# Kernel tuning notes

Measured on AMD Instinct MI355X. Metric: run time of the kernel, lower is better.

## Reference

```python
import jax, jax.numpy as jnp
import numpy as np

N = 16384
IN_DIM = 512
HID = 256
E = 262144


def setup_inputs() -> dict:
    key = jax.random.key(0)
    k1, k2, k3, k4, k5, k6 = jax.random.split(key, 6)
    # Xavier-uniform-like init scale for the weights
    lim1 = float(np.sqrt(6.0 / (IN_DIM + HID)))
    lim2 = float(np.sqrt(6.0 / (HID + 1)))
    return {
        "X": jax.random.normal(k1, (N, IN_DIM), dtype=jnp.float32),
        "adj": jax.random.uniform(k2, (N, N), dtype=jnp.float32),
        "weight": jax.random.uniform(k3, (IN_DIM, HID), dtype=jnp.float32, minval=-lim1, maxval=lim1),
        "weight_two": jax.random.uniform(k4, (HID, 1), dtype=jnp.float32, minval=-lim2, maxval=lim2),
        "train_edges": jax.random.randint(k5, (E, 2), 0, N, dtype=jnp.int64 if jax.config.read("jax_enable_x64") else jnp.int32),
        "train_false_edges": jax.random.randint(k6, (E, 2), 0, N, dtype=jnp.int64 if jax.config.read("jax_enable_x64") else jnp.int32),
    }


def reference(X, adj, weight, weight_two, train_edges, train_false_edges):
    # encode: Z = adj @ (X @ W)
    Z = adj @ (X @ weight)  # [N, HID]
    # decode: per-edge gather + elementwise multiply + small linear + sigmoid
    edges = jnp.concatenate([train_edges, train_false_edges], axis=0)  # [2E, 2]
    z_i = Z[edges[:, 0]]  # [2E, HID]
    z_j = Z[edges[:, 1]]  # [2E, HID]
    logits = (z_i * z_j) @ weight_two  # [2E, 1]
    return jax.nn.sigmoid(logits)
```

## Files before the change

kernel.cpp:

```cpp
#include <hip/hip_runtime.h>
#include <math.h>


typedef _Float16 half8v __attribute__((ext_vector_type(8)));
typedef __attribute__((ext_vector_type(4))) float floatx4;

#define NM_ (16384L * 256L)
#define KT 256

static __device__ __forceinline__ void split2_pair_f16(float x0, float x1,
                                                       unsigned& q1, unsigned& q2) {
  _Float16 h0 = (_Float16)x0, h1 = (_Float16)x1;
  float r0 = x0 - (float)h0, r1 = x1 - (float)h1;
  _Float16 g0 = (_Float16)r0, g1 = (_Float16)r1;
  q1 = ((unsigned)__builtin_bit_cast(unsigned short, h1) << 16) |
       __builtin_bit_cast(unsigned short, h0);
  q2 = ((unsigned)__builtin_bit_cast(unsigned short, g1) << 16) |
       __builtin_bit_cast(unsigned short, g0);
}

#define BM 128
#define BN 128
#define BK 16
#define LDAS (BM + 4)
#define LDBS (BN + 4)

__global__ __launch_bounds__(256, 1)
void gemm_f32_nn(const float* __restrict__ A, const float* __restrict__ B,
                 float* __restrict__ C, int M, int N, int K)
{
  __shared__ float As[2][BK][LDAS];
  __shared__ float Bs[2][BK][LDBS];

  const int tid = threadIdx.x;
  const int tx = tid & 15;
  const int ty = tid >> 4;
  const long m0 = (long)blockIdx.x * BM;
  const long n0 = (long)blockIdx.y * BN;

  const int a_row = tid >> 2;
  const int a_kc  = (tid & 3) << 2;
  const int b_row = tid >> 5;
  const int b_col = (tid & 31) << 2;

  const float* Ag0 = A + (m0 + a_row) * (long)K + a_kc;
  const float* Ag1 = A + (m0 + 64 + a_row) * (long)K + a_kc;
  const float* Bg0 = B + (long)b_row * N + n0 + b_col;
  const float* Bg1 = B + (long)(b_row + 8) * N + n0 + b_col;

  float4 av0 = *(const float4*)(Ag0);
  float4 av1 = *(const float4*)(Ag1);
  float4 bv0 = *(const float4*)(Bg0);
  float4 bv1 = *(const float4*)(Bg1);

  float acc[8][8];
#pragma unroll
  for (int i = 0; i < 8; ++i)
#pragma unroll
    for (int j = 0; j < 8; ++j) acc[i][j] = 0.f;

  const int nt = K / BK;
  int buf = 0;

#pragma unroll
  for (int i = 0; i < 4; ++i) {
    As[0][a_kc + i][a_row]      = (&av0.x)[i];
    As[0][a_kc + i][a_row + 64] = (&av1.x)[i];
  }
  *(float4*)&Bs[0][b_row][b_col]     = bv0;
  *(float4*)&Bs[0][b_row + 8][b_col] = bv1;
  __syncthreads();

  for (int t = 0; t < nt; ++t) {
    if (t + 1 < nt) {
      const long ko = (long)(t + 1) * BK;
      av0 = *(const float4*)(Ag0 + ko);
      av1 = *(const float4*)(Ag1 + ko);
      bv0 = *(const float4*)(Bg0 + ko * N);
      bv1 = *(const float4*)(Bg1 + ko * N);
    }
    float tacc[8][8];
#pragma unroll
    for (int i = 0; i < 8; ++i)
#pragma unroll
      for (int j = 0; j < 8; ++j) tacc[i][j] = 0.f;

#pragma unroll
    for (int kk = 0; kk < BK; ++kk) {
      float4 aA = *(const float4*)&As[buf][kk][ty * 4];
      float4 aB = *(const float4*)&As[buf][kk][ty * 4 + 64];
      float4 bA = *(const float4*)&Bs[buf][kk][tx * 4];
      float4 bB = *(const float4*)&Bs[buf][kk][tx * 4 + 64];
      const float ar[8] = {aA.x, aA.y, aA.z, aA.w, aB.x, aB.y, aB.z, aB.w};
      const float br[8] = {bA.x, bA.y, bA.z, bA.w, bB.x, bB.y, bB.z, bB.w};
#pragma unroll
      for (int i = 0; i < 8; ++i)
#pragma unroll
        for (int j = 0; j < 8; ++j)
          tacc[i][j] = fmaf(ar[i], br[j], tacc[i][j]);
    }
#pragma unroll
    for (int i = 0; i < 8; ++i)
#pragma unroll
      for (int j = 0; j < 8; ++j) acc[i][j] += tacc[i][j];

    if (t + 1 < nt) {
      const int nb = buf ^ 1;
#pragma unroll
      for (int i = 0; i < 4; ++i) {
        As[nb][a_kc + i][a_row]      = (&av0.x)[i];
        As[nb][a_kc + i][a_row + 64] = (&av1.x)[i];
      }
      *(float4*)&Bs[nb][b_row][b_col]     = bv0;
      *(float4*)&Bs[nb][b_row + 8][b_col] = bv1;
    }
    __syncthreads();
    buf ^= 1;
  }

#pragma unroll
  for (int i = 0; i < 8; ++i) {
    const long row = m0 + (i < 4 ? ty * 4 + i : 64 + ty * 4 + (i - 4));
#pragma unroll
    for (int c = 0; c < 2; ++c) {
      float4 v;
      v.x = acc[i][c * 4 + 0];
      v.y = acc[i][c * 4 + 1];
      v.z = acc[i][c * 4 + 2];
      v.w = acc[i][c * 4 + 3];
      *(float4*)&C[row * N + n0 + tx * 4 + c * 64] = v;
    }
  }
}

__global__ __launch_bounds__(256)
void transpose_split(const float* __restrict__ XW,
                     unsigned short* __restrict__ X1,
                     unsigned short* __restrict__ X2)
{
  __shared__ float T[64][65];
  const int tid = threadIdx.x;
  const long kb = (long)blockIdx.x * 64;
  const long nb = (long)blockIdx.y * 64;

#pragma unroll
  for (int i = 0; i < 4; ++i) {
    int idx = tid + 256 * i;
    int r = idx >> 4, c4 = (idx & 15) * 4;
    float4 v = *(const float4*)&XW[(kb + r) * 256 + nb + c4];
    T[r][c4 + 0] = v.x; T[r][c4 + 1] = v.y; T[r][c4 + 2] = v.z; T[r][c4 + 3] = v.w;
  }
  __syncthreads();

#pragma unroll
  for (int i = 0; i < 2; ++i) {
    int idx = tid + 256 * i;
    int n = idx >> 3, kq = (idx & 7) * 8;
    float x[8];
#pragma unroll
    for (int j = 0; j < 8; ++j) x[j] = T[kq + j][n];
    unsigned q1[4], q2[4];
#pragma unroll
    for (int p = 0; p < 4; ++p)
      split2_pair_f16(x[2 * p], x[2 * p + 1], q1[p], q2[p]);
    const long gk = kb + kq;
    const long gt = gk >> 5;
    const int  c  = (int)((gk >> 3) & 3);
    const long o  = ((gt * 4 + c) * 256 + (nb + n)) * 8;
    *(uint4*)&X1[o] = make_uint4(q1[0], q1[1], q1[2], q1[3]);
    *(uint4*)&X2[o] = make_uint4(q2[0], q2[1], q2[2], q2[3]);
  }
}


__global__ __launch_bounds__(256, 2)
void gemm_split2(const float* __restrict__ A,
                 const unsigned short* __restrict__ Bg,
                 float* __restrict__ P0, float* __restrict__ P1)
{
  __shared__ unsigned short As[2][8192];

  const int tid  = threadIdx.x;
  const int lane = tid & 63;
  const int w    = tid >> 6;
  const int wm   = w >> 1, wn = w & 1;

  const int bid = blockIdx.x;
  const int swz = (bid & 7) * 64 + (bid >> 3);
  const long m0 = (long)(swz >> 2) * 128;
  const long n0 = (long)((swz >> 1) & 1) * 128;
  const int  z  = swz & 1;
  float* __restrict__ Cp = z ? P1 : P0;

  const int arow = tid & 127;
  const int ah   = tid >> 7;
  const float* Ag = A + (m0 + arow) * 16384L + (long)z * 8192 + ah * 16;

  int awr[2][2];
#pragma unroll
  for (int s = 0; s < 2; ++s)
#pragma unroll
    for (int q = 0; q < 2; ++q)
      awr[s][q] = ((s * 4 + 2 * ah + q) * 128 + arow) * 8;

  const int fr = lane & 15;
  const int kc = lane >> 4;

  const unsigned short* Bq = Bg + (long)kc * 2048 + ((long)n0 + wn * 64 + fr) * 8;

  floatx4 acc[4][4], accS[4][4];
#pragma unroll
  for (int i = 0; i < 4; ++i)
#pragma unroll
    for (int j = 0; j < 4; ++j) { acc[i][j] = (floatx4)0.f; accS[i][j] = (floatx4)0.f; }

  float4  pa[4];
  half8v  bf[2][4];

#define SPLIT_WRITE(NB)                                                           \
  {                                                                               \
    unsigned q1[8], q2[8];                                                        \
    _Pragma("unroll")                                                             \
    for (int p = 0; p < 8; ++p) {                                                 \
      float x0 = (&pa[p >> 1].x)[(2 * p) & 3];                                    \
      float x1 = (&pa[p >> 1].x)[(2 * p + 1) & 3];                                \
      split2_pair_f16(x0, x1, q1[p], q2[p]);                                      \
    }                                                                             \
    *(uint4*)&As[NB][awr[0][0]] = make_uint4(q1[0], q1[1], q1[2], q1[3]);         \
    *(uint4*)&As[NB][awr[0][1]] = make_uint4(q1[4], q1[5], q1[6], q1[7]);         \
    *(uint4*)&As[NB][awr[1][0]] = make_uint4(q2[0], q2[1], q2[2], q2[3]);         \
    *(uint4*)&As[NB][awr[1][1]] = make_uint4(q2[4], q2[5], q2[6], q2[7]);         \
  }

#define LOAD_BF(TILE)                                                             \
  {                                                                               \
    const long bo_ = ((long)z * KT + (TILE)) * 8192;                              \
    _Pragma("unroll")                                                             \
    for (int s = 0; s < 2; ++s)                                                   \
      _Pragma("unroll")                                                           \
      for (int fn = 0; fn < 4; ++fn)                                              \
        bf[s][fn] = *(const half8v*)(Bq + s * NM_ + bo_ + fn * 128);              \
  }

#define BODY(TT, CUR)                                                             \
  {                                                                               \
    SPLIT_WRITE((CUR) ^ 1);                                                       \
    {                                                                             \
      const long ko_ = (long)(((TT) + 2) & (KT - 1)) * 32;                        \
      _Pragma("unroll")                                                           \
      for (int i = 0; i < 4; ++i) pa[i] = *(const float4*)(Ag + ko_ + i * 4);     \
    }                                                                             \
    _Pragma("unroll")                                                             \
    for (int fm = 0; fm < 4; ++fm) {                                              \
      const int ar_ = (wm * 64 + fm * 16 + fr) * 8;                               \
      half8v af0 = *(const half8v*)&As[CUR][kc * 1024 + ar_];                     \
      half8v af1 = *(const half8v*)&As[CUR][(4 + kc) * 1024 + ar_];               \
      _Pragma("unroll")                                                           \
      for (int fn = 0; fn < 4; ++fn) {                                            \
        floatx4 d = acc[fm][fn];                                                  \
        d = __builtin_amdgcn_mfma_f32_16x16x32_f16(af0, bf[0][fn], d, 0, 0, 0);   \
        d = __builtin_amdgcn_mfma_f32_16x16x32_f16(af0, bf[1][fn], d, 0, 0, 0);   \
        d = __builtin_amdgcn_mfma_f32_16x16x32_f16(af1, bf[0][fn], d, 0, 0, 0);   \
        acc[fm][fn] = d;                                                          \
      }                                                                           \
    }                                                                             \
    LOAD_BF(((TT) + 1) & (KT - 1));                                               \
    if (((TT) & 31) == 31) {                                                      \
      _Pragma("unroll")                                                           \
      for (int i = 0; i < 4; ++i)                                                 \
        _Pragma("unroll")                                                         \
        for (int j = 0; j < 4; ++j) { accS[i][j] += acc[i][j]; acc[i][j] = (floatx4)0.f; } \
    }                                                                             \
    asm volatile("s_waitcnt lgkmcnt(0)" ::: "memory");                            \
    __builtin_amdgcn_s_barrier();                                                 \
    __builtin_amdgcn_sched_barrier(0);                                            \
  }

#pragma unroll
  for (int i = 0; i < 4; ++i) pa[i] = *(const float4*)(Ag + i * 4);
  LOAD_BF(0);
  SPLIT_WRITE(0);
#pragma unroll
  for (int i = 0; i < 4; ++i) pa[i] = *(const float4*)(Ag + 32 + i * 4);
  asm volatile("s_waitcnt lgkmcnt(0)" ::: "memory");
  __builtin_amdgcn_s_barrier();
  __builtin_amdgcn_sched_barrier(0);

  for (int t = 0; t < KT; t += 2) {
    BODY(t,     0);
    BODY(t + 1, 1);
  }

#pragma unroll
  for (int fm = 0; fm < 4; ++fm) {
#pragma unroll
    for (int fn = 0; fn < 4; ++fn) {
      const long col  = n0 + wn * 64 + fn * 16 + fr;
      const long rowb = m0 + wm * 64 + fm * 16 + (lane >> 4) * 4;
#pragma unroll
      for (int j = 0; j < 4; ++j)
        Cp[(rowb + j) * 256 + col] = accS[fm][fn][j];
    }
  }
#undef BODY
#undef LOAD_BF
#undef SPLIT_WRITE
}

__global__ __launch_bounds__(256)
void reduce_add(const float* __restrict__ P0, float* __restrict__ P1, long n4)
{
  long i = (long)blockIdx.x * 256 + threadIdx.x;
  const long stride = (long)gridDim.x * 256;
  for (; i < n4; i += stride) {
    float4 a = ((const float4*)P0)[i];
    float4 b = ((const float4*)P1)[i];
    b.x += a.x; b.y += a.y; b.z += a.z; b.w += a.w;
    ((float4*)P1)[i] = b;
  }
}

__global__ __launch_bounds__(256)
void edge_score(const float* __restrict__ Z, const float* __restrict__ w2,
                const int* __restrict__ te, const int* __restrict__ fe,
                int E, float* __restrict__ out)
{
  const long gtid = (long)blockIdx.x * 256 + threadIdx.x;
  const long wid = gtid >> 6;
  const int lane = threadIdx.x & 63;
  if (wid >= 2L * E) return;
  const int* ep = (wid < E) ? (te + 2 * wid) : (fe + 2 * (wid - E));
  const int src = ep[0];
  const int dst = ep[1];
  const float4 a = ((const float4*)(Z + (long)src * 256))[lane];
  const float4 b = ((const float4*)(Z + (long)dst * 256))[lane];
  const float4 w = ((const float4*)w2)[lane];
  float s = a.x * b.x * w.x + a.y * b.y * w.y + a.z * b.z * w.z + a.w * b.w * w.w;
#pragma unroll
  for (int off = 32; off > 0; off >>= 1) s += __shfl_down(s, off);
  if (lane == 0) out[wid] = 1.0f / (1.0f + expf(-s));
}

extern "C" void kernel_launch(void* const* d_in, const int* in_sizes, int n_in,
                              void* d_out, int out_size, void* d_ws, size_t ws_size,
                              hipStream_t stream)
{
  const float* X   = (const float*)d_in[0];
  const float* adj = (const float*)d_in[1];
  const float* W   = (const float*)d_in[2];
  const float* W2  = (const float*)d_in[3];
  const int*   te  = (const int*)d_in[4];
  const int*   fe  = (const int*)d_in[5];

  const int E = in_sizes[4] / 2;

  float* ws = (float*)d_ws;
  float* XW = ws;
  float* P0 = ws;
  float* P1 = ws + NM_;
  unsigned short* X1 = (unsigned short*)(ws + 2 * NM_);
  unsigned short* X2 = X1 + NM_;

  dim3 blk(256);
  gemm_f32_nn<<<dim3(128, 2), blk, 0, stream>>>(X, W, XW, 16384, 256, 512);
  transpose_split<<<dim3(256, 4), blk, 0, stream>>>(XW, X1, X2);
  gemm_split2<<<dim3(512), blk, 0, stream>>>(adj, X1, P0, P1);
  reduce_add<<<dim3(2048), blk, 0, stream>>>(P0, P1, NM_ / 4);
  const long nwaves = 2L * E;
  const int nblocks = (int)((nwaves + 3) / 4);
  edge_score<<<dim3(nblocks), blk, 0, stream>>>(P1, W2, te, fe, E, (float*)d_out);
}
```

Measured before the change: 767.2 us.

## Use split-fp16 MFMA for X@W and restructure adj GEMM without LDS

Replaces the FP32 SIMT GEMM for X@W with a split-fp16 MFMA kernel, fed by a new kernel that pre-splits W into hi/lo fp16 halves. The adj GEMM is rebuilt so each 512-thread block covers all 256 output columns. Each wave loads and splits its own A fragments directly from global memory into registers, with no LDS staging or barriers. This removes shared-memory traffic and syncs and reads each adj row tile once per K-half. The trade-off is that lanes load A fragments with strided, less coalesced accesses, and register pressure rises.

```diff
diff --git a/kernel.cpp b/kernel.cpp
--- a/kernel.cpp
+++ b/kernel.cpp
@@ -3,10 +3,10 @@
 
 
 typedef _Float16 half8v __attribute__((ext_vector_type(8)));
+typedef __fp16   fp16x2 __attribute__((ext_vector_type(2)));
 typedef __attribute__((ext_vector_type(4))) float floatx4;
 
 #define NM_ (16384L * 256L)
-#define KT 256
 
 static __device__ __forceinline__ void split2_pair_f16(float x0, float x1,
                                                        unsigned& q1, unsigned& q2) {
@@ -19,118 +19,99 @@
        __builtin_bit_cast(unsigned short, g0);
 }
 
-#define BM 128
-#define BN 128
-#define BK 16
-#define LDAS (BM + 4)
-#define LDBS (BN + 4)
-
-__global__ __launch_bounds__(256, 1)
-void gemm_f32_nn(const float* __restrict__ A, const float* __restrict__ B,
-                 float* __restrict__ C, int M, int N, int K)
-{
-  __shared__ float As[2][BK][LDAS];
-  __shared__ float Bs[2][BK][LDBS];
-
-  const int tid = threadIdx.x;
-  const int tx = tid & 15;
-  const int ty = tid >> 4;
-  const long m0 = (long)blockIdx.x * BM;
-  const long n0 = (long)blockIdx.y * BN;
-
-  const int a_row = tid >> 2;
-  const int a_kc  = (tid & 3) << 2;
-  const int b_row = tid >> 5;
-  const int b_col = (tid & 31) << 2;
-
-  const float* Ag0 = A + (m0 + a_row) * (long)K + a_kc;
-  const float* Ag1 = A + (m0 + 64 + a_row) * (long)K + a_kc;
-  const float* Bg0 = B + (long)b_row * N + n0 + b_col;
-  const float* Bg1 = B + (long)(b_row + 8) * N + n0 + b_col;
-
-  float4 av0 = *(const float4*)(Ag0);
-  float4 av1 = *(const float4*)(Ag1);
-  float4 bv0 = *(const float4*)(Bg0);
-  float4 bv1 = *(const float4*)(Bg1);
-
-  float acc[8][8];
-#pragma unroll
-  for (int i = 0; i < 8; ++i)
-#pragma unroll
-    for (int j = 0; j < 8; ++j) acc[i][j] = 0.f;
-
-  const int nt = K / BK;
-  int buf = 0;
-
-#pragma unroll
-  for (int i = 0; i < 4; ++i) {
-    As[0][a_kc + i][a_row]      = (&av0.x)[i];
-    As[0][a_kc + i][a_row + 64] = (&av1.x)[i];
-  }
-  *(float4*)&Bs[0][b_row][b_col]     = bv0;
-  *(float4*)&Bs[0][b_row + 8][b_col] = bv1;
-  __syncthreads();
-
-  for (int t = 0; t < nt; ++t) {
-    if (t + 1 < nt) {
-      const long ko = (long)(t + 1) * BK;
-      av0 = *(const float4*)(Ag0 + ko);
-      av1 = *(const float4*)(Ag1 + ko);
-      bv0 = *(const float4*)(Bg0 + ko * N);
-      bv1 = *(const float4*)(Bg1 + ko * N);
-    }
-    float tacc[8][8];
-#pragma unroll
-    for (int i = 0; i < 8; ++i)
-#pragma unroll
-      for (int j = 0; j < 8; ++j) tacc[i][j] = 0.f;
-
-#pragma unroll
-    for (int kk = 0; kk < BK; ++kk) {
-      float4 aA = *(const float4*)&As[buf][kk][ty * 4];
-      float4 aB = *(const float4*)&As[buf][kk][ty * 4 + 64];
-      float4 bA = *(const float4*)&Bs[buf][kk][tx * 4];
-      float4 bB = *(const float4*)&Bs[buf][kk][tx * 4 + 64];
-      const float ar[8] = {aA.x, aA.y, aA.z, aA.w, aB.x, aB.y, aB.z, aB.w};
-      const float br[8] = {bA.x, bA.y, bA.z, bA.w, bB.x, bB.y, bB.z, bB.w};
-#pragma unroll
-      for (int i = 0; i < 8; ++i)
-#pragma unroll
-        for (int j = 0; j < 8; ++j)
-          tacc[i][j] = fmaf(ar[i], br[j], tacc[i][j]);
-    }
-#pragma unroll
-    for (int i = 0; i < 8; ++i)
-#pragma unroll
-      for (int j = 0; j < 8; ++j) acc[i][j] += tacc[i][j];
-
-    if (t + 1 < nt) {
-      const int nb = buf ^ 1;
-#pragma unroll
-      for (int i = 0; i < 4; ++i) {
-        As[nb][a_kc + i][a_row]      = (&av0.x)[i];
-        As[nb][a_kc + i][a_row + 64] = (&av1.x)[i];
+static __device__ __forceinline__ void split8(const float* __restrict__ x,
+                                              half8v& a0, half8v& a1) {
+  union U { unsigned u[4]; half8v h; } u0, u1;
+#pragma unroll
+  for (int p = 0; p < 4; ++p) {
+    fp16x2 h = __builtin_amdgcn_cvt_pkrtz(x[2 * p], x[2 * p + 1]);
+    float r0 = x[2 * p]     - (float)h[0];
+    float r1 = x[2 * p + 1] - (float)h[1];
+    fp16x2 g = __builtin_amdgcn_cvt_pkrtz(r0, r1);
+    u0.u[p] = __builtin_bit_cast(unsigned, h);
+    u1.u[p] = __builtin_bit_cast(unsigned, g);
+  }
+  a0 = u0.h; a1 = u1.h;
+}
+
+__global__ __launch_bounds__(256)
+void w_split(const float* __restrict__ W, unsigned short* __restrict__ WT)
+{
+  const int b  = blockIdx.x;
+  const int kt = b >> 2, c = b & 3;
+  const int n  = threadIdx.x;
+  const int k0 = kt * 32 + c * 8;
+  float x[8];
+#pragma unroll
+  for (int j = 0; j < 8; ++j) x[j] = W[(k0 + j) * 256 + n];
+  unsigned q1[4], q2[4];
+#pragma unroll
+  for (int p = 0; p < 4; ++p)
+    split2_pair_f16(x[2 * p], x[2 * p + 1], q1[p], q2[p]);
+  const long o = ((long)(kt * 4 + c) * 256 + n) * 8;
+  *(uint4*)&WT[o]          = make_uint4(q1[0], q1[1], q1[2], q1[3]);
+  *(uint4*)&WT[o + 131072] = make_uint4(q2[0], q2[1], q2[2], q2[3]);
+}
+
+__global__ __launch_bounds__(256, 2)
+void gemm_xw(const float* __restrict__ X, const unsigned short* __restrict__ WT,
+             float* __restrict__ XW)
+{
+  const int tid  = threadIdx.x;
+  const int lane = tid & 63;
+  const int w    = tid >> 6;
+  const int wm = w >> 1, wn = w & 1;
+  const long m0 = (long)(blockIdx.x >> 1) * 128;
+  const long n0 = (long)(blockIdx.x & 1) * 128;
+  const int fr = lane & 15, kc = lane >> 4;
+
+  const unsigned short* Bq = WT + (long)kc * 2048 + ((long)n0 + wn * 64 + fr) * 8;
+
+  const float* ap[4];
+#pragma unroll
+  for (int fm = 0; fm < 4; ++fm)
+    ap[fm] = X + (m0 + wm * 64 + fm * 16 + fr) * 512L + kc * 8;
+
+  floatx4 acc[4][4];
+#pragma unroll
+  for (int i = 0; i < 4; ++i)
+#pragma unroll
+    for (int j = 0; j < 4; ++j) acc[i][j] = (floatx4)0.f;
+
+  for (int t = 0; t < 16; ++t) {
+    half8v bf0[4], bf1[4];
+#pragma unroll
+    for (int fn = 0; fn < 4; ++fn) {
+      bf0[fn] = *(const half8v*)(Bq + (long)t * 8192 + fn * 128);
+      bf1[fn] = *(const half8v*)(Bq + (long)t * 8192 + fn * 128 + 131072);
+    }
+#pragma unroll
+    for (int fm = 0; fm < 4; ++fm) {
+      float x[8];
+      *(float4*)&x[0] = *(const float4*)(ap[fm] + t * 32);
+      *(float4*)&x[4] = *(const float4*)(ap[fm] + t * 32 + 4);
+      half8v a0, a1;
+      split8(x, a0, a1);
+#pragma unroll
+      for (int fn = 0; fn < 4; ++fn) {
+        floatx4 d = acc[fm][fn];
+        d = __builtin_amdgcn_mfma_f32_16x16x32_f16(a0, bf0[fn], d, 0, 0, 0);
+        d = __builtin_amdgcn_mfma_f32_16x16x32_f16(a0, bf1[fn], d, 0, 0, 0);
+        d = __builtin_amdgcn_mfma_f32_16x16x32_f16(a1, bf0[fn], d, 0, 0, 0);
+        acc[fm][fn] = d;
       }
-      *(float4*)&Bs[nb][b_row][b_col]     = bv0;
-      *(float4*)&Bs[nb][b_row + 8][b_col] = bv1;
-    }
-    __syncthreads();
-    buf ^= 1;
-  }
-
-#pragma unroll
-  for (int i = 0; i < 8; ++i) {
-    const long row = m0 + (i < 4 ? ty * 4 + i : 64 + ty * 4 + (i - 4));
-#pragma unroll
-    for (int c = 0; c < 2; ++c) {
-      float4 v;
-      v.x = acc[i][c * 4 + 0];
-      v.y = acc[i][c * 4 + 1];
-      v.z = acc[i][c * 4 + 2];
-      v.w = acc[i][c * 4 + 3];
-      *(float4*)&C[row * N + n0 + tx * 4 + c * 64] = v;
-    }
-  }
+    }
+  }
+#pragma unroll
+  for (int fm = 0; fm < 4; ++fm)
+#pragma unroll
+    for (int fn = 0; fn < 4; ++fn) {
+      const long col  = n0 + wn * 64 + fn * 16 + fr;
+      const long rowb = m0 + wm * 64 + fm * 16 + kc * 4;
+#pragma unroll
+      for (int j = 0; j < 4; ++j)
+        XW[(rowb + j) * 256 + col] = acc[fm][fn][j];
+    }
 }
 
 __global__ __launch_bounds__(256)
@@ -172,41 +153,28 @@
   }
 }
 
-
-__global__ __launch_bounds__(256, 2)
-void gemm_split2(const float* __restrict__ A,
-                 const unsigned short* __restrict__ Bg,
-                 float* __restrict__ P0, float* __restrict__ P1)
-{
-  __shared__ unsigned short As[2][8192];
-
+__global__ __launch_bounds__(512, 2)
+void gemm_adj(const float* __restrict__ A, const unsigned short* __restrict__ Bg,
+              float* __restrict__ P0, float* __restrict__ P1)
+{
   const int tid  = threadIdx.x;
   const int lane = tid & 63;
   const int w    = tid >> 6;
-  const int wm   = w >> 1, wn = w & 1;
-
+  const int wm = w >> 2, wn = w & 3;
   const int bid = blockIdx.x;
-  const int swz = (bid & 7) * 64 + (bid >> 3);
-  const long m0 = (long)(swz >> 2) * 128;
-  const long n0 = (long)((swz >> 1) & 1) * 128;
-  const int  z  = swz & 1;
+  const long m0 = (long)(bid & 127) * 128;
+  const int  z  = bid >> 7;
   float* __restrict__ Cp = z ? P1 : P0;
-
-  const int arow = tid & 127;
-  const int ah   = tid >> 7;
-  const float* Ag = A + (m0 + arow) * 16384L + (long)z * 8192 + ah * 16;
-
-  int awr[2][2];
-#pragma unroll
-  for (int s = 0; s < 2; ++s)
-#pragma unroll
-    for (int q = 0; q < 2; ++q)
-      awr[s][q] = ((s * 4 + 2 * ah + q) * 128 + arow) * 8;
-
-  const int fr = lane & 15;
-  const int kc = lane >> 4;
-
-  const unsigned short* Bq = Bg + (long)kc * 2048 + ((long)n0 + wn * 64 + fr) * 8;
+  const int fr = lane & 15, kc = lane >> 4;
+
+  const unsigned short* Bq0 = Bg + (long)z * 2097152 + (long)kc * 2048 +
+                              ((long)wn * 64 + fr) * 8;
+  const unsigned short* Bq1 = Bq0 + NM_;
+
+  const float* ap[4];
+#pragma unroll
+  for (int fm = 0; fm < 4; ++fm)
+    ap[fm] = A + (m0 + wm * 64 + fm * 16 + fr) * 16384L + (long)z * 8192 + kc * 8;
 
   floatx4 acc[4][4], accS[4][4];
 #pragma unroll
@@ -214,97 +182,61 @@
 #pragma unroll
     for (int j = 0; j < 4; ++j) { acc[i][j] = (floatx4)0.f; accS[i][j] = (floatx4)0.f; }
 
-  float4  pa[4];
-  half8v  bf[2][4];
-
-#define SPLIT_WRITE(NB)                                                           \
-  {                                                                               \
-    unsigned q1[8], q2[8];                                                        \
-    _Pragma("unroll")                                                             \
-    for (int p = 0; p < 8; ++p) {                                                 \
-      float x0 = (&pa[p >> 1].x)[(2 * p) & 3];                                    \
-      float x1 = (&pa[p >> 1].x)[(2 * p + 1) & 3];                                \
-      split2_pair_f16(x0, x1, q1[p], q2[p]);                                      \
-    }                                                                             \
-    *(uint4*)&As[NB][awr[0][0]] = make_uint4(q1[0], q1[1], q1[2], q1[3]);         \
-    *(uint4*)&As[NB][awr[0][1]] = make_uint4(q1[4], q1[5], q1[6], q1[7]);         \
-    *(uint4*)&As[NB][awr[1][0]] = make_uint4(q2[0], q2[1], q2[2], q2[3]);         \
-    *(uint4*)&As[NB][awr[1][1]] = make_uint4(q2[4], q2[5], q2[6], q2[7]);         \
-  }
-
-#define LOAD_BF(TILE)                                                             \
-  {                                                                               \
-    const long bo_ = ((long)z * KT + (TILE)) * 8192;                              \
-    _Pragma("unroll")                                                             \
-    for (int s = 0; s < 2; ++s)                                                   \
-      _Pragma("unroll")                                                           \
-      for (int fn = 0; fn < 4; ++fn)                                              \
-        bf[s][fn] = *(const half8v*)(Bq + s * NM_ + bo_ + fn * 128);              \
-  }
-
-#define BODY(TT, CUR)                                                             \
-  {                                                                               \
-    SPLIT_WRITE((CUR) ^ 1);                                                       \
-    {                                                                             \
-      const long ko_ = (long)(((TT) + 2) & (KT - 1)) * 32;                        \
-      _Pragma("unroll")                                                           \
-      for (int i = 0; i < 4; ++i) pa[i] = *(const float4*)(Ag + ko_ + i * 4);     \
-    }                                                                             \
-    _Pragma("unroll")                                                             \
-    for (int fm = 0; fm < 4; ++fm) {                                              \
-      const int ar_ = (wm * 64 + fm * 16 + fr) * 8;                               \
-      half8v af0 = *(const half8v*)&As[CUR][kc * 1024 + ar_];                     \
-      half8v af1 = *(const half8v*)&As[CUR][(4 + kc) * 1024 + ar_];               \
-      _Pragma("unroll")                                                           \
-      for (int fn = 0; fn < 4; ++fn) {                                            \
-        floatx4 d = acc[fm][fn];                                                  \
-        d = __builtin_amdgcn_mfma_f32_16x16x32_f16(af0, bf[0][fn], d, 0, 0, 0);   \
-        d = __builtin_amdgcn_mfma_f32_16x16x32_f16(af0, bf[1][fn], d, 0, 0, 0);   \
-        d = __builtin_amdgcn_mfma_f32_16x16x32_f16(af1, bf[0][fn], d, 0, 0, 0);   \
-        acc[fm][fn] = d;                                                          \
-      }                                                                           \
-    }                                                                             \
-    LOAD_BF(((TT) + 1) & (KT - 1));                                               \
-    if (((TT) & 31) == 31) {                                                      \
-      _Pragma("unroll")                                                           \
-      for (int i = 0; i < 4; ++i)                                                 \
-        _Pragma("unroll")                                                         \
-        for (int j = 0; j < 4; ++j) { accS[i][j] += acc[i][j]; acc[i][j] = (floatx4)0.f; } \
-    }                                                                             \
-    asm volatile("s_waitcnt lgkmcnt(0)" ::: "memory");                            \
-    __builtin_amdgcn_s_barrier();                                                 \
-    __builtin_amdgcn_sched_barrier(0);                                            \
-  }
-
-#pragma unroll
-  for (int i = 0; i < 4; ++i) pa[i] = *(const float4*)(Ag + i * 4);
-  LOAD_BF(0);
-  SPLIT_WRITE(0);
-#pragma unroll
-  for (int i = 0; i < 4; ++i) pa[i] = *(const float4*)(Ag + 32 + i * 4);
-  asm volatile("s_waitcnt lgkmcnt(0)" ::: "memory");
-  __builtin_amdgcn_s_barrier();
-  __builtin_amdgcn_sched_barrier(0);
-
-  for (int t = 0; t < KT; t += 2) {
-    BODY(t,     0);
-    BODY(t + 1, 1);
-  }
+  float  ra[4][8];
+  half8v bf0[4], bf1[4];
 
 #pragma unroll
   for (int fm = 0; fm < 4; ++fm) {
+    *(float4*)&ra[fm][0] = *(const float4*)(ap[fm]);
+    *(float4*)&ra[fm][4] = *(const float4*)(ap[fm] + 4);
+  }
+#pragma unroll
+  for (int fn = 0; fn < 4; ++fn) {
+    bf0[fn] = *(const half8v*)(Bq0 + fn * 128);
+    bf1[fn] = *(const half8v*)(Bq1 + fn * 128);
+  }
+
+  for (int t = 0; t < 256; ++t) {
+    const long ko = (long)((t + 1) & 255) * 32;
+    const long bo = (long)((t + 1) & 255) * 8192;
+#pragma unroll
+    for (int fm = 0; fm < 4; ++fm) {
+      half8v a0, a1;
+      split8(ra[fm], a0, a1);
+      *(float4*)&ra[fm][0] = *(const float4*)(ap[fm] + ko);
+      *(float4*)&ra[fm][4] = *(const float4*)(ap[fm] + ko + 4);
+#pragma unroll
+      for (int fn = 0; fn < 4; ++fn) {
+        floatx4 d = acc[fm][fn];
+        d = __builtin_amdgcn_mfma_f32_16x16x32_f16(a0, bf0[fn], d, 0, 0, 0);
+        d = __builtin_amdgcn_mfma_f32_16x16x32_f16(a0, bf1[fn], d, 0, 0, 0);
+        d = __builtin_amdgcn_mfma_f32_16x16x32_f16(a1, bf0[fn], d, 0, 0, 0);
+        acc[fm][fn] = d;
+      }
+    }
 #pragma unroll
     for (int fn = 0; fn < 4; ++fn) {
-      const long col  = n0 + wn * 64 + fn * 16 + fr;
-      const long rowb = m0 + wm * 64 + fm * 16 + (lane >> 4) * 4;
+      bf0[fn] = *(const half8v*)(Bq0 + bo + fn * 128);
+      bf1[fn] = *(const half8v*)(Bq1 + bo + fn * 128);
+    }
+    if ((t & 31) == 31) {
+#pragma unroll
+      for (int i = 0; i < 4; ++i)
+#pragma unroll
+        for (int j = 0; j < 4; ++j) { accS[i][j] += acc[i][j]; acc[i][j] = (floatx4)0.f; }
+    }
+  }
+
+#pragma unroll
+  for (int fm = 0; fm < 4; ++fm)
+#pragma unroll
+    for (int fn = 0; fn < 4; ++fn) {
+      const long col  = wn * 64 + fn * 16 + fr;
+      const long rowb = m0 + wm * 64 + fm * 16 + kc * 4;
 #pragma unroll
       for (int j = 0; j < 4; ++j)
         Cp[(rowb + j) * 256 + col] = accS[fm][fn][j];
     }
-  }
-#undef BODY
-#undef LOAD_BF
-#undef SPLIT_WRITE
 }
 
 __global__ __launch_bounds__(256)
@@ -355,18 +287,19 @@
   const int E = in_sizes[4] / 2;
 
   float* ws = (float*)d_ws;
-  float* XW = ws;
   float* P0 = ws;
   float* P1 = ws + NM_;
   unsigned short* X1 = (unsigned short*)(ws + 2 * NM_);
   unsigned short* X2 = X1 + NM_;
-
-  dim3 blk(256);
-  gemm_f32_nn<<<dim3(128, 2), blk, 0, stream>>>(X, W, XW, 16384, 256, 512);
-  transpose_split<<<dim3(256, 4), blk, 0, stream>>>(XW, X1, X2);
-  gemm_split2<<<dim3(512), blk, 0, stream>>>(adj, X1, P0, P1);
-  reduce_add<<<dim3(2048), blk, 0, stream>>>(P0, P1, NM_ / 4);
+  unsigned short* WT = X2 + NM_;
+
+  dim3 b256(256);
+  w_split<<<dim3(64), b256, 0, stream>>>(W, WT);
+  gemm_xw<<<dim3(256), b256, 0, stream>>>(X, WT, P0);
+  transpose_split<<<dim3(256, 4), b256, 0, stream>>>(P0, X1, X2);
+  gemm_adj<<<dim3(256), dim3(512), 0, stream>>>(adj, X1, P0, P1);
+  reduce_add<<<dim3(2048), b256, 0, stream>>>(P0, P1, NM_ / 4);
   const long nwaves = 2L * E;
   const int nblocks = (int)((nwaves + 3) / 4);
-  edge_score<<<dim3(nblocks), blk, 0, stream>>>(P1, W2, te, fe, E, (float*)d_out);
-}
+  edge_score<<<dim3(nblocks), b256, 0, stream>>>(P1, W2, te, fe, E, (float*)d_out);
+}
```

Result: slower. 835.8 us (+8.9%).
